# Optimization experiments

Hardware: AMD Instinct MI355X
Metric: run time of the kernel (lower is better)

The kernel has to match this reference:

```python
import jax, jax.numpy as jnp
import numpy as np

CONF_THRES = 0.45
IOU_THRES = 0.45
K = 1000      # candidate cap after confidence filtering (top-K by score)
MAX_DET = 300 # max detections kept per image


def setup_inputs() -> dict:
    key = jax.random.key(0)
    k1, k2 = jax.random.split(key)
    B, N, NC = 16, 25200, 80
    p = jax.random.uniform(k1, (B, N, 5 + NC), dtype=jnp.float32)
    # scale xywh to realistic pixel coords: cx,cy in [0,640), w,h in [0,128)
    scale = jnp.concatenate([jnp.array([640.0, 640.0, 128.0, 128.0], jnp.float32),
                             jnp.ones((1 + NC,), jnp.float32)])
    prediction = p * scale
    logits = jax.random.normal(k2, (B, N, NC), dtype=jnp.float32)
    return {"prediction": prediction, "logits": logits}


def xywh2xyxy(x):
    cx, cy, w, h = x[..., 0], x[..., 1], x[..., 2], x[..., 3]
    return jnp.stack([cx - w / 2, cy - h / 2, cx + w / 2, cy + h / 2], axis=-1)


def box_iou(a, b):
    # a: [K,4], b: [K,4] in xyxy -> [K,K]
    area_a = (a[:, 2] - a[:, 0]) * (a[:, 3] - a[:, 1])
    area_b = (b[:, 2] - b[:, 0]) * (b[:, 3] - b[:, 1])
    lt = jnp.maximum(a[:, None, :2], b[None, :, :2])
    rb = jnp.minimum(a[:, None, 2:], b[None, :, 2:])
    wh = jnp.clip(rb - lt, 0.0)
    inter = wh[..., 0] * wh[..., 1]
    return inter / (area_a[:, None] + area_b[None, :] - inter + 1e-9)


def _nms_image(pred, log):
    # pred: [N, 5+nc], log: [N, nc]
    obj = pred[:, 4]
    cls_scores = pred[:, 5:] * obj[:, None]          # x[:,5:] *= x[:,4:5]
    conf = jnp.max(cls_scores, axis=-1)
    j = jnp.argmax(cls_scores, axis=-1)
    box = xywh2xyxy(pred[:, :4])
    valid = (obj > CONF_THRES) & (conf > CONF_THRES)
    score = jnp.where(valid, conf, -1.0)
    sc, idx = jax.lax.top_k(score, K)                # descending, as torchvision nms sorts
    b = box[idx]                                     # [K,4]
    c = j[idx]                                       # [K]
    lg = log[idx]                                    # [K,nc]
    v = sc > 0.0
    iou = box_iou(b, b)                              # [K,K]
    ar = jnp.arange(K)

    def body(i, state):
        keep, supp = state
        alive = jnp.logical_not(supp[i])
        keep = keep.at[i].set(alive)
        supp = supp | (alive & (iou[i] > IOU_THRES) & (ar > i))
        return keep, supp

    keep, _ = jax.lax.fori_loop(0, K, body, (jnp.zeros((K,), bool), jnp.logical_not(v)))
    ksc = jnp.where(keep, sc, -1.0)
    fsc, fidx = jax.lax.top_k(ksc, MAX_DET)
    m = fsc > 0.0                                    # validity mask per detection row
    det = jnp.concatenate([b[fidx], sc[fidx][:, None], c[fidx].astype(jnp.float32)[:, None]], axis=1)
    det = jnp.where(m[:, None], det, 0.0)            # padded rows = zeros((0,6)) analogue
    lgo = jnp.where(m[:, None], lg[fidx], 0.0)
    return det, m, lgo


def reference(prediction, logits):
    # det: [B, MAX_DET, 6] (x1,y1,x2,y2,conf,cls), mask: [B, MAX_DET], logits_out: [B, MAX_DET, nc]
    det, mask, logits_out = jax.vmap(_nms_image)(prediction, logits)
    return det, mask, logits_out
```

## Files before the change

kernel.cpp:

```cpp
#include <hip/hip_runtime.h>
#include <hip/hip_bf16.h>

#define BATCH 16
#define NCAND 25200
#define NCLS 80
#define PREDC 85
#define KTOP 1000
#define MAXDET 300
#define CAP 2048
#define NBINS 1024
#define TILE_ROWS 128
#define CONF 0.45f
#define HSCALE ((float)NBINS / (1.0f - 0.45f))
#define CNT_STRIDE 16

typedef unsigned long long ull;

__global__ __launch_bounds__(256) void k_init(int* __restrict__ hist,
                                              ull* __restrict__ keys,
                                              int* __restrict__ cnt) {
    int t = blockIdx.x * 256 + threadIdx.x;
    keys[t] = ~0ULL;
    if (t < BATCH * NBINS) hist[t] = 0;
    if (t < BATCH * CNT_STRIDE) cnt[t] = 0;
}

__global__ __launch_bounds__(256) void k_score(const float* __restrict__ pred,
                                               float* __restrict__ score,
                                               float* __restrict__ bx,
                                               int* __restrict__ cls,
                                               int* __restrict__ hist) {
    __shared__ float lds[TILE_ROWS * PREDC];
    int tile = blockIdx.x;
    int tid = threadIdx.x;
    size_t base = (size_t)tile * (TILE_ROWS * PREDC);
    const float4* src4 = (const float4*)(pred + base);
    float4* l4 = (float4*)lds;
    const int NV4 = TILE_ROWS * PREDC / 4;
    for (int k = tid; k < NV4; k += 256) l4[k] = src4[k];
    __syncthreads();
    if (tid < TILE_ROWS) {
        const float* row = lds + tid * PREDC;
        float obj = row[4];
        float best = -1.0f; int bj = 0;
        #pragma unroll 8
        for (int c = 0; c < NCLS; ++c) {
            float v = row[5 + c] * obj;
            if (v > best) { best = v; bj = c; }
        }
        bool valid = (obj > CONF) && (best > CONF);
        float s = valid ? best : -1.0f;
        int grow = tile * TILE_ROWS + tid;
        score[grow] = s;
        cls[grow] = bj;
        float cx = row[0], cy = row[1], w = row[2], h = row[3];
        ((float4*)bx)[grow] = make_float4(cx - w * 0.5f, cy - h * 0.5f,
                                          cx + w * 0.5f, cy + h * 0.5f);
        if (s > CONF) {
            int b = grow / NCAND;
            int bin = (int)((s - CONF) * HSCALE);
            bin = bin < 0 ? 0 : (bin > NBINS - 1 ? NBINS - 1 : bin);
            atomicAdd(&hist[b * NBINS + bin], 1);
        }
    }
}

__global__ __launch_bounds__(256) void k_findT(const int* __restrict__ hist,
                                               int* __restrict__ Tarr) {
    int b = blockIdx.x, tid = threadIdx.x;
    __shared__ int h[NBINS];
    __shared__ int s_T;
    if (tid == 0) s_T = 0;
    #pragma unroll
    for (int k = 0; k < 4; ++k) h[tid + k * 256] = hist[b * NBINS + tid + k * 256];
    __syncthreads();
    for (int off = 1; off < NBINS; off <<= 1) {
        int tmp[4];
        #pragma unroll
        for (int k = 0; k < 4; ++k) {
            int idx = tid + k * 256;
            tmp[k] = (idx + off < NBINS) ? h[idx + off] : 0;
        }
        __syncthreads();
        #pragma unroll
        for (int k = 0; k < 4; ++k) h[tid + k * 256] += tmp[k];
        __syncthreads();
    }
    #pragma unroll
    for (int k = 0; k < 4; ++k) {
        int idx = tid + k * 256;
        int S = h[idx];
        int Sn = (idx + 1 < NBINS) ? h[idx + 1] : 0;
        if (S >= KTOP && Sn < KTOP) s_T = idx;
    }
    __syncthreads();
    if (tid == 0) Tarr[b] = s_T;
}

__global__ __launch_bounds__(256) void k_gather(const float* __restrict__ score,
                                                const int* __restrict__ Tarr,
                                                ull* __restrict__ keys,
                                                int* __restrict__ cnt) {
    int b = blockIdx.y;
    int n = blockIdx.x * 256 + threadIdx.x;
    int tid = threadIdx.x;
    __shared__ int wbase[4];
    __shared__ int sT;
    if (tid == 0) sT = Tarr[b];
    __syncthreads();
    bool want = false;
    float s = 0.0f;
    if (n < NCAND) {
        s = score[b * NCAND + n];
        if (s > CONF) {
            int bin = (int)((s - CONF) * HSCALE);
            bin = bin < 0 ? 0 : (bin > NBINS - 1 ? NBINS - 1 : bin);
            want = (bin >= sT);
        }
    }
    ull m = __ballot(want);
    int lane = tid & 63, widx = tid >> 6;
    if (lane == 0) wbase[widx] = __popcll(m);
    __syncthreads();
    if (tid == 0) {
        int t0 = wbase[0], t1 = wbase[1], t2 = wbase[2], t3 = wbase[3];
        int tot = t0 + t1 + t2 + t3;
        int b0 = tot ? atomicAdd(&cnt[b * CNT_STRIDE], tot) : 0;
        wbase[0] = b0; wbase[1] = b0 + t0; wbase[2] = b0 + t0 + t1; wbase[3] = b0 + t0 + t1 + t2;
    }
    __syncthreads();
    if (want) {
        int pos = wbase[widx] + __popcll(m & ((1ULL << lane) - 1ULL));
        if (pos < CAP) {
            unsigned int sb = __float_as_uint(s);
            keys[b * CAP + pos] = ((ull)(~sb) << 32) | (unsigned)n;
        }
    }
}

__global__ __launch_bounds__(1024) void k_sort(const float* __restrict__ bx,
                                               const int* __restrict__ cls,
                                               const ull* __restrict__ keys,
                                               const int* __restrict__ cnt,
                                               int* __restrict__ topidx,
                                               float* __restrict__ topsc,
                                               int* __restrict__ topcls,
                                               float* __restrict__ boxes) {
    int b = blockIdx.x, tid = threadIdx.x;
    __shared__ ull sbuf[CAP];
    __shared__ int s_C2;
    if (tid == 0) {
        int c = cnt[b * CNT_STRIDE];
        s_C2 = c > CAP ? CAP : c;
    }
    __syncthreads();
    int C2 = s_C2;
    unsigned P = (C2 <= 1024) ? 1024u : 2048u;
    sbuf[tid] = keys[b * CAP + tid];
    if (P > 1024) sbuf[tid + 1024] = keys[b * CAP + tid + 1024];
    __syncthreads();
    for (unsigned k = 2; k <= P; k <<= 1) {
        for (unsigned j = k >> 1; j > 0; j >>= 1) {
            for (unsigned t = tid; t < P; t += 1024) {
                unsigned ixj = t ^ j;
                if (ixj > t) {
                    ull a = sbuf[t], bb = sbuf[ixj];
                    if ((a > bb) == ((t & k) == 0)) { sbuf[t] = bb; sbuf[ixj] = a; }
                }
            }
            __syncthreads();
        }
    }
    if (tid < KTOP) {
        int o = b * KTOP + tid;
        if (tid < C2) {
            ull key = sbuf[tid];
            int n = (int)(key & 0xFFFFFFFFULL);
            float s = __uint_as_float(~(unsigned int)(key >> 32));
            topidx[o] = n;
            topsc[o] = s;
            topcls[o] = cls[b * NCAND + n];
            ((float4*)boxes)[o] = ((const float4*)bx)[b * NCAND + n];
        } else {
            topidx[o] = 0; topsc[o] = -1.0f; topcls[o] = 0;
            ((float4*)boxes)[o] = make_float4(0.f, 0.f, 0.f, 0.f);
        }
    }
}

__global__ __launch_bounds__(256) void k_iou(const float* __restrict__ boxes,
                                             ull* __restrict__ M) {
    #pragma clang fp contract(off)
    int g = blockIdx.x * 256 + threadIdx.x;
    int w = g & 15;
    int bi = g >> 4;
    int i = bi % KTOP;
    int b = bi / KTOP;
    int j0 = w * 64;
    if (j0 + 63 <= i) {
        M[(size_t)bi * 16 + w] = 0ULL;
        return;
    }
    const float4* bxp = (const float4*)boxes + (size_t)b * KTOP;
    float4 A = bxp[i];
    float areaA = (A.z - A.x) * (A.w - A.y);
    ull word = 0;
    int jend = j0 + 64; if (jend > KTOP) jend = KTOP;
    #pragma unroll 4
    for (int j = j0; j < jend; ++j) {
        float4 Bb = bxp[j];
        float areaB = (Bb.z - Bb.x) * (Bb.w - Bb.y);
        float lx = fmaxf(A.x, Bb.x), ly = fmaxf(A.y, Bb.y);
        float rx = fminf(A.z, Bb.z), ry = fminf(A.w, Bb.w);
        float ww = rx - lx; ww = ww > 0.f ? ww : 0.f;
        float hh = ry - ly; hh = hh > 0.f ? hh : 0.f;
        float inter = ww * hh;
        float denom = ((areaA + areaB) - inter) + 1e-9f;
        float iou = inter / denom;
        if (j > i && iou > 0.45f) word |= 1ULL << (j - j0);
    }
    M[(size_t)bi * 16 + w] = word;
}

__global__ __launch_bounds__(1024) void k_nms_out(const ull* __restrict__ M,
                                                  const int* __restrict__ cnt,
                                                  const float* __restrict__ logits,
                                                  const int* __restrict__ topidx,
                                                  const float* __restrict__ topsc,
                                                  const int* __restrict__ topcls,
                                                  const float* __restrict__ boxes,
                                                  float* __restrict__ out) {
    __shared__ ull buf[2][64 * 17];
    __shared__ ull s_keep[16];
    __shared__ int kept_r[MAXDET];
    __shared__ int kept_n[MAXDET];
    __shared__ int s_kc;
    int b = blockIdx.x, tid = threadIdx.x;
    int kc0 = cnt[b * CNT_STRIDE]; if (kc0 > KTOP) kc0 = KTOP;
    const ull* Mb = M + (size_t)b * KTOP * 16;
    buf[0][(tid >> 4) * 17 + (tid & 15)] = Mb[tid];
    __syncthreads();
    ull supp;
    {
        int w = tid & 15, lo = w * 64;
        if (kc0 <= lo) supp = ~0ULL;
        else if (kc0 >= lo + 64) supp = 0ULL;
        else supp = (~0ULL) << (kc0 - lo);
    }
    for (int rb = 0; rb < 16; ++rb) {
        int cur = rb & 1, nxt = cur ^ 1;
        if (tid >= 64) {
            if (rb < 15) {
                for (int u = tid - 64; u < 1024; u += 960) {
                    int idx = (rb + 1) * 1024 + u;
                    int g = idx < 16000 ? idx : 15999;
                    buf[nxt][(u >> 4) * 17 + (u & 15)] = Mb[g];
                }
            }
        } else {
            int l = tid, w = l & 15, q = l >> 4;
            const ull* B = buf[cur];
            ull drow = B[l * 17 + rb];
            ull crow[16];
            #pragma unroll
            for (int k = 0; k < 16; ++k) crow[k] = B[(q + 4 * k) * 17 + w];
            int slo = (int)(supp & 0xffffffffULL);
            int shi = (int)(supp >> 32);
            unsigned rlo = (unsigned)__builtin_amdgcn_readlane(slo, rb)
                         | (unsigned)__builtin_amdgcn_readlane(slo, rb + 16)
                         | (unsigned)__builtin_amdgcn_readlane(slo, rb + 32)
                         | (unsigned)__builtin_amdgcn_readlane(slo, rb + 48);
            unsigned rhi = (unsigned)__builtin_amdgcn_readlane(shi, rb)
                         | (unsigned)__builtin_amdgcn_readlane(shi, rb + 16)
                         | (unsigned)__builtin_amdgcn_readlane(shi, rb + 32)
                         | (unsigned)__builtin_amdgcn_readlane(shi, rb + 48);
            ull removed = ((ull)rhi << 32) | rlo;
            int dlo_v = (int)(drow & 0xffffffffULL);
            int dhi_v = (int)(drow >> 32);
            #pragma unroll
            for (int s = 0; s < 64; ++s) {
                unsigned dl = (unsigned)__builtin_amdgcn_readlane(dlo_v, s);
                unsigned dh = (unsigned)__builtin_amdgcn_readlane(dhi_v, s);
                ull d64 = ((ull)dh << 32) | dl;
                if (!((removed >> s) & 1ULL)) removed |= d64;
            }
            ull acc = 0;
            #pragma unroll
            for (int k = 0; k < 16; ++k) {
                int r = q + 4 * k;
                if (!((removed >> r) & 1ULL)) acc |= crow[k];
            }
            supp |= acc;
        }
        __syncthreads();
    }
    if (tid < 64) {
        supp |= __shfl_xor(supp, 16);
        supp |= __shfl_xor(supp, 32);
        if (tid < 16) s_keep[tid] = ~supp;
    }
    __syncthreads();
    if (tid < 16) {
        int pre = 0;
        for (int u = 0; u < tid; ++u) pre += __popcll(s_keep[u]);
        ull wv = s_keep[tid];
        int rank = pre;
        while (wv) {
            int bit = __builtin_ctzll(wv);
            if (rank < MAXDET) kept_r[rank] = tid * 64 + bit;
            rank++;
            wv &= wv - 1;
        }
        if (tid == 15) s_kc = rank < MAXDET ? rank : MAXDET;
    }
    __syncthreads();
    int kc = s_kc;
    if (tid < MAXDET && tid < kc) kept_n[tid] = topidx[b * KTOP + kept_r[tid]];
    __syncthreads();
    float* det = out;
    float* mask_o = out + BATCH * MAXDET * 6;
    float* lgo = out + BATCH * MAXDET * 6 + BATCH * MAXDET;
    for (int idx = tid; idx < MAXDET * 6; idx += 1024) {
        int s = idx / 6, col = idx % 6;
        float v = 0.f;
        if (s < kc) {
            int o = b * KTOP + kept_r[s];
            if (col < 4) v = boxes[o * 4 + col];
            else if (col == 4) v = topsc[o];
            else v = (float)topcls[o];
        }
        det[b * MAXDET * 6 + idx] = v;
    }
    for (int s = tid; s < MAXDET; s += 1024)
        mask_o[b * MAXDET + s] = (s < kc) ? 1.0f : 0.0f;
    float4* lgo4 = (float4*)(lgo + (size_t)b * MAXDET * NCLS);
    const float4* lg4 = (const float4*)logits;
    for (int idx = tid; idx < MAXDET * (NCLS / 4); idx += 1024) {
        int s = idx / (NCLS / 4), cc = idx % (NCLS / 4);
        float4 v = make_float4(0.f, 0.f, 0.f, 0.f);
        if (s < kc) v = lg4[((size_t)b * NCAND + kept_n[s]) * (NCLS / 4) + cc];
        lgo4[idx] = v;
    }
}

extern "C" void kernel_launch(void* const* d_in, const int* in_sizes, int n_in,
                              void* d_out, int out_size, void* d_ws, size_t ws_size,
                              hipStream_t stream) {
    (void)in_sizes; (void)n_in; (void)out_size; (void)ws_size;
    const float* pred = (const float*)d_in[0];
    const float* logits = (const float*)d_in[1];
    float* out = (float*)d_out;
    char* ws = (char*)d_ws;

    float* score  = (float*)(ws + 0);
    int*   hist   = (int*)(ws + 1612800);
    int*   Tarr   = (int*)(ws + 1678336);
    ull*   M      = (ull*)(ws + 0);
    ull*   keys   = (ull*)(ws + 2048000);
    int*   cnt    = (int*)(ws + 2310144);
    int*   topidx = (int*)(ws + 2311168);
    float* topsc  = (float*)(ws + 2375168);
    int*   topcls = (int*)(ws + 2439168);
    float* boxes  = (float*)(ws + 2503168);
    float* bx     = (float*)(ws + 2759168);
    int*   cls    = (int*)(ws + 9210368);

    const int nrows = BATCH * NCAND;
    k_init<<<128, 256, 0, stream>>>(hist, keys, cnt);
    k_score<<<nrows / TILE_ROWS, 256, 0, stream>>>(pred, score, bx, cls, hist);
    k_findT<<<BATCH, 256, 0, stream>>>(hist, Tarr);
    k_gather<<<dim3((NCAND + 255) / 256, BATCH), 256, 0, stream>>>(score, Tarr, keys, cnt);
    k_sort<<<BATCH, 1024, 0, stream>>>(bx, cls, keys, cnt, topidx, topsc, topcls, boxes);
    k_iou<<<(BATCH * KTOP * 16) / 256, 256, 0, stream>>>(boxes, M);
    k_nms_out<<<BATCH, 1024, 0, stream>>>(M, cnt, logits, topidx, topsc, topcls, boxes, out);
}
```

Baseline: 143.2 us.

## Fuse histogram, threshold, gather and sort into one per-image top-k kernel

Replaces four kernels (init, global-atomic histogram, threshold finding, gather) plus the shared-memory sort with a single per-image kernel. It builds the histogram in shared memory, finds the threshold, compacts candidates into LDS with wave-level atomics, and runs a register-resident bitonic sort that uses cross-lane shuffles for small strides. This removes launch overhead, global atomics and intermediate global buffers. The cost is only 16 blocks scanning 25200 scores each twice, which could limit parallelism in the scan phases.

```diff
diff --git a/kernel.cpp b/kernel.cpp
--- a/kernel.cpp
+++ b/kernel.cpp
@@ -16,20 +16,10 @@
 
 typedef unsigned long long ull;
 
-__global__ __launch_bounds__(256) void k_init(int* __restrict__ hist,
-                                              ull* __restrict__ keys,
-                                              int* __restrict__ cnt) {
-    int t = blockIdx.x * 256 + threadIdx.x;
-    keys[t] = ~0ULL;
-    if (t < BATCH * NBINS) hist[t] = 0;
-    if (t < BATCH * CNT_STRIDE) cnt[t] = 0;
-}
-
 __global__ __launch_bounds__(256) void k_score(const float* __restrict__ pred,
                                                float* __restrict__ score,
                                                float* __restrict__ bx,
-                                               int* __restrict__ cls,
-                                               int* __restrict__ hist) {
+                                               int* __restrict__ cls) {
     __shared__ float lds[TILE_ROWS * PREDC];
     int tile = blockIdx.x;
     int tid = threadIdx.x;
@@ -56,127 +46,151 @@
         float cx = row[0], cy = row[1], w = row[2], h = row[3];
         ((float4*)bx)[grow] = make_float4(cx - w * 0.5f, cy - h * 0.5f,
                                           cx + w * 0.5f, cy + h * 0.5f);
-        if (s > CONF) {
-            int b = grow / NCAND;
-            int bin = (int)((s - CONF) * HSCALE);
-            bin = bin < 0 ? 0 : (bin > NBINS - 1 ? NBINS - 1 : bin);
-            atomicAdd(&hist[b * NBINS + bin], 1);
-        }
-    }
-}
-
-__global__ __launch_bounds__(256) void k_findT(const int* __restrict__ hist,
-                                               int* __restrict__ Tarr) {
-    int b = blockIdx.x, tid = threadIdx.x;
-    __shared__ int h[NBINS];
-    __shared__ int s_T;
-    if (tid == 0) s_T = 0;
-    #pragma unroll
-    for (int k = 0; k < 4; ++k) h[tid + k * 256] = hist[b * NBINS + tid + k * 256];
-    __syncthreads();
-    for (int off = 1; off < NBINS; off <<= 1) {
-        int tmp[4];
-        #pragma unroll
-        for (int k = 0; k < 4; ++k) {
-            int idx = tid + k * 256;
-            tmp[k] = (idx + off < NBINS) ? h[idx + off] : 0;
-        }
-        __syncthreads();
-        #pragma unroll
-        for (int k = 0; k < 4; ++k) h[tid + k * 256] += tmp[k];
-        __syncthreads();
-    }
-    #pragma unroll
-    for (int k = 0; k < 4; ++k) {
-        int idx = tid + k * 256;
-        int S = h[idx];
-        int Sn = (idx + 1 < NBINS) ? h[idx + 1] : 0;
-        if (S >= KTOP && Sn < KTOP) s_T = idx;
-    }
-    __syncthreads();
-    if (tid == 0) Tarr[b] = s_T;
-}
-
-__global__ __launch_bounds__(256) void k_gather(const float* __restrict__ score,
-                                                const int* __restrict__ Tarr,
-                                                ull* __restrict__ keys,
-                                                int* __restrict__ cnt) {
-    int b = blockIdx.y;
-    int n = blockIdx.x * 256 + threadIdx.x;
-    int tid = threadIdx.x;
-    __shared__ int wbase[4];
-    __shared__ int sT;
-    if (tid == 0) sT = Tarr[b];
-    __syncthreads();
-    bool want = false;
-    float s = 0.0f;
-    if (n < NCAND) {
-        s = score[b * NCAND + n];
-        if (s > CONF) {
-            int bin = (int)((s - CONF) * HSCALE);
-            bin = bin < 0 ? 0 : (bin > NBINS - 1 ? NBINS - 1 : bin);
-            want = (bin >= sT);
-        }
-    }
-    ull m = __ballot(want);
-    int lane = tid & 63, widx = tid >> 6;
-    if (lane == 0) wbase[widx] = __popcll(m);
-    __syncthreads();
-    if (tid == 0) {
-        int t0 = wbase[0], t1 = wbase[1], t2 = wbase[2], t3 = wbase[3];
-        int tot = t0 + t1 + t2 + t3;
-        int b0 = tot ? atomicAdd(&cnt[b * CNT_STRIDE], tot) : 0;
-        wbase[0] = b0; wbase[1] = b0 + t0; wbase[2] = b0 + t0 + t1; wbase[3] = b0 + t0 + t1 + t2;
-    }
-    __syncthreads();
-    if (want) {
-        int pos = wbase[widx] + __popcll(m & ((1ULL << lane) - 1ULL));
-        if (pos < CAP) {
-            unsigned int sb = __float_as_uint(s);
-            keys[b * CAP + pos] = ((ull)(~sb) << 32) | (unsigned)n;
-        }
-    }
-}
-
-__global__ __launch_bounds__(1024) void k_sort(const float* __restrict__ bx,
+    }
+}
+
+__device__ __forceinline__ void cmpx(ull& r, ull p, bool keepMin) {
+    ull mn = r < p ? r : p;
+    ull mx = r < p ? p : r;
+    r = keepMin ? mn : mx;
+}
+
+__global__ __launch_bounds__(1024) void k_topk(const float* __restrict__ score,
+                                               const float* __restrict__ bx,
                                                const int* __restrict__ cls,
-                                               const ull* __restrict__ keys,
-                                               const int* __restrict__ cnt,
                                                int* __restrict__ topidx,
                                                float* __restrict__ topsc,
                                                int* __restrict__ topcls,
-                                               float* __restrict__ boxes) {
+                                               float* __restrict__ boxes,
+                                               int* __restrict__ cnt) {
+    __shared__ int hist[NBINS];
+    __shared__ ull sbuf[CAP];
+    __shared__ int s_T, s_base;
     int b = blockIdx.x, tid = threadIdx.x;
-    __shared__ ull sbuf[CAP];
-    __shared__ int s_C2;
-    if (tid == 0) {
-        int c = cnt[b * CNT_STRIDE];
-        s_C2 = c > CAP ? CAP : c;
-    }
-    __syncthreads();
-    int C2 = s_C2;
-    unsigned P = (C2 <= 1024) ? 1024u : 2048u;
-    sbuf[tid] = keys[b * CAP + tid];
-    if (P > 1024) sbuf[tid + 1024] = keys[b * CAP + tid + 1024];
-    __syncthreads();
-    for (unsigned k = 2; k <= P; k <<= 1) {
+    int lane = tid & 63;
+    const float* sc = score + (size_t)b * NCAND;
+    const float4* sc4 = (const float4*)sc;
+    const int NF4 = NCAND / 4;
+    hist[tid] = 0;
+    if (tid == 0) { s_T = 0; s_base = 0; }
+    __syncthreads();
+    for (int f = tid; f < NF4; f += 1024) {
+        float4 v4 = sc4[f];
+        float vs[4] = {v4.x, v4.y, v4.z, v4.w};
+        #pragma unroll
+        for (int e = 0; e < 4; ++e) {
+            float s = vs[e];
+            if (s > CONF) {
+                int bin = (int)((s - CONF) * HSCALE);
+                bin = bin < 0 ? 0 : (bin > NBINS - 1 ? NBINS - 1 : bin);
+                atomicAdd(&hist[bin], 1);
+            }
+        }
+    }
+    __syncthreads();
+    for (int off = 1; off < NBINS; off <<= 1) {
+        int v = (tid + off < NBINS) ? hist[tid + off] : 0;
+        __syncthreads();
+        hist[tid] += v;
+        __syncthreads();
+    }
+    {
+        int S = hist[tid];
+        int Sn = (tid + 1 < NBINS) ? hist[tid + 1] : 0;
+        if (S >= KTOP && Sn < KTOP) s_T = tid;
+    }
+    sbuf[tid] = ~0ULL;
+    sbuf[tid + 1024] = ~0ULL;
+    __syncthreads();
+    int T = s_T;
+    for (int f = tid; f < NF4; f += 1024) {
+        float4 v4 = sc4[f];
+        float vs[4] = {v4.x, v4.y, v4.z, v4.w};
+        #pragma unroll
+        for (int e = 0; e < 4; ++e) {
+            float s = vs[e];
+            bool want = false;
+            if (s > CONF) {
+                int bin = (int)((s - CONF) * HSCALE);
+                bin = bin < 0 ? 0 : (bin > NBINS - 1 ? NBINS - 1 : bin);
+                want = (bin >= T);
+            }
+            ull m = __ballot(want);
+            int wb = 0;
+            if (lane == 0 && m) wb = atomicAdd(&s_base, (int)__popcll(m));
+            wb = __shfl(wb, 0);
+            if (want) {
+                int pos = wb + (int)__popcll(m & ((1ULL << lane) - 1ULL));
+                if (pos < CAP) {
+                    unsigned sb2 = __float_as_uint(s);
+                    sbuf[pos] = ((ull)(~sb2) << 32) | (unsigned)(f * 4 + e);
+                }
+            }
+        }
+    }
+    __syncthreads();
+    int C2 = s_base; if (C2 > CAP) C2 = CAP;
+    ull r0 = sbuf[tid];
+    ull r1 = sbuf[tid + 1024];
+    int t2 = tid + 1024;
+    #pragma unroll
+    for (unsigned k = 2; k <= 64; k <<= 1) {
+        #pragma unroll
         for (unsigned j = k >> 1; j > 0; j >>= 1) {
-            for (unsigned t = tid; t < P; t += 1024) {
-                unsigned ixj = t ^ j;
-                if (ixj > t) {
-                    ull a = sbuf[t], bb = sbuf[ixj];
-                    if ((a > bb) == ((t & k) == 0)) { sbuf[t] = bb; sbuf[ixj] = a; }
-                }
-            }
+            ull p0 = __shfl_xor(r0, (int)j);
+            ull p1 = __shfl_xor(r1, (int)j);
+            bool amLow = ((tid & j) == 0);
+            cmpx(r0, p0, amLow == ((tid & k) == 0));
+            cmpx(r1, p1, amLow == ((t2 & k) == 0));
+        }
+    }
+    #pragma unroll
+    for (unsigned k = 128; k <= 1024; k <<= 1) {
+        #pragma unroll
+        for (unsigned j = k >> 1; j >= 64; j >>= 1) {
+            sbuf[tid] = r0; sbuf[t2] = r1;
             __syncthreads();
+            ull p0 = sbuf[tid ^ j];
+            ull p1 = sbuf[t2 ^ j];
+            cmpx(r0, p0, ((tid & j) == 0) == ((tid & k) == 0));
+            cmpx(r1, p1, ((t2 & j) == 0) == ((t2 & k) == 0));
+            __syncthreads();
+        }
+        #pragma unroll
+        for (unsigned j = 32; j > 0; j >>= 1) {
+            ull p0 = __shfl_xor(r0, (int)j);
+            ull p1 = __shfl_xor(r1, (int)j);
+            bool amLow = ((tid & j) == 0);
+            cmpx(r0, p0, amLow == ((tid & k) == 0));
+            cmpx(r1, p1, amLow == ((t2 & k) == 0));
+        }
+    }
+    {
+        if (r1 < r0) { ull t = r0; r0 = r1; r1 = t; }
+        #pragma unroll
+        for (unsigned j = 512; j >= 64; j >>= 1) {
+            sbuf[tid] = r0; sbuf[t2] = r1;
+            __syncthreads();
+            ull p0 = sbuf[tid ^ j];
+            ull p1 = sbuf[t2 ^ j];
+            cmpx(r0, p0, ((tid & j) == 0));
+            cmpx(r1, p1, ((t2 & j) == 0));
+            __syncthreads();
+        }
+        #pragma unroll
+        for (unsigned j = 32; j > 0; j >>= 1) {
+            ull p0 = __shfl_xor(r0, (int)j);
+            ull p1 = __shfl_xor(r1, (int)j);
+            bool amLow = ((tid & j) == 0);
+            cmpx(r0, p0, amLow);
+            cmpx(r1, p1, amLow);
         }
     }
     if (tid < KTOP) {
         int o = b * KTOP + tid;
         if (tid < C2) {
-            ull key = sbuf[tid];
-            int n = (int)(key & 0xFFFFFFFFULL);
-            float s = __uint_as_float(~(unsigned int)(key >> 32));
+            int n = (int)(r0 & 0xFFFFFFFFULL);
+            float s = __uint_as_float(~(unsigned)(r0 >> 32));
             topidx[o] = n;
             topsc[o] = s;
             topcls[o] = cls[b * NCAND + n];
@@ -186,6 +200,7 @@
             ((float4*)boxes)[o] = make_float4(0.f, 0.f, 0.f, 0.f);
         }
     }
+    if (tid == 0) cnt[b * CNT_STRIDE] = C2;
 }
 
 __global__ __launch_bounds__(256) void k_iou(const float* __restrict__ boxes,
@@ -353,24 +368,18 @@
     char* ws = (char*)d_ws;
 
     float* score  = (float*)(ws + 0);
-    int*   hist   = (int*)(ws + 1612800);
-    int*   Tarr   = (int*)(ws + 1678336);
+    float* bx     = (float*)(ws + 1612800);
+    int*   cls    = (int*)(ws + 8064000);
     ull*   M      = (ull*)(ws + 0);
-    ull*   keys   = (ull*)(ws + 2048000);
-    int*   cnt    = (int*)(ws + 2310144);
-    int*   topidx = (int*)(ws + 2311168);
-    float* topsc  = (float*)(ws + 2375168);
-    int*   topcls = (int*)(ws + 2439168);
-    float* boxes  = (float*)(ws + 2503168);
-    float* bx     = (float*)(ws + 2759168);
-    int*   cls    = (int*)(ws + 9210368);
+    int*   cnt    = (int*)(ws + 9676800);
+    int*   topidx = (int*)(ws + 9677824);
+    float* topsc  = (float*)(ws + 9741824);
+    int*   topcls = (int*)(ws + 9805824);
+    float* boxes  = (float*)(ws + 9869824);
 
     const int nrows = BATCH * NCAND;
-    k_init<<<128, 256, 0, stream>>>(hist, keys, cnt);
-    k_score<<<nrows / TILE_ROWS, 256, 0, stream>>>(pred, score, bx, cls, hist);
-    k_findT<<<BATCH, 256, 0, stream>>>(hist, Tarr);
-    k_gather<<<dim3((NCAND + 255) / 256, BATCH), 256, 0, stream>>>(score, Tarr, keys, cnt);
-    k_sort<<<BATCH, 1024, 0, stream>>>(bx, cls, keys, cnt, topidx, topsc, topcls, boxes);
+    k_score<<<nrows / TILE_ROWS, 256, 0, stream>>>(pred, score, bx, cls);
+    k_topk<<<BATCH, 1024, 0, stream>>>(score, bx, cls, topidx, topsc, topcls, boxes, cnt);
     k_iou<<<(BATCH * KTOP * 16) / 256, 256, 0, stream>>>(boxes, M);
     k_nms_out<<<BATCH, 1024, 0, stream>>>(M, cnt, logits, topidx, topsc, topcls, boxes, out);
 }
```

Measured after the change: 131.2 us. 1.09x faster.
